# Optimization experiments

Hardware: AMD Instinct MI355X
Metric: run time of the kernel (lower is better)

Reference implementation:

```python
import jax, jax.numpy as jnp
import numpy as np

NUM_NEG_PAIRS = 64
NUM_NEG_INDICES_FOR_LOSS = 16
B, C, H, W = 1, 64, 768, 768
HW = H * W


def setup_inputs() -> dict:
    key = jax.random.key(0)
    k1, k2, k3, k4 = jax.random.split(key, 4)
    feats1 = jax.random.normal(k1, (B, C, H, W), dtype=jnp.float32)
    feats2 = jax.random.normal(k2, (B, C, H, W), dtype=jnp.float32)
    positive_pairs = jax.random.randint(k3, (64, 2), 0, HW, dtype=jnp.int64 if jax.config.jax_enable_x64 else jnp.int32)
    negative_indices = jax.random.randint(k4, (NUM_NEG_PAIRS,), 0, HW, dtype=jnp.int64 if jax.config.jax_enable_x64 else jnp.int32)
    return {"feats1": feats1, "feats2": feats2,
            "positive_pairs": positive_pairs,
            "negative_indices": negative_indices}


def reference(feats1, feats2, positive_pairs, negative_indices):
    # feats1/feats2: [1, C, H, W] -> flatten to [C, HW] (matches .view(C, -1) with B=1)
    f1 = feats1.reshape(C, -1)
    f2 = feats2.reshape(C, -1)
    sel = f1[:, negative_indices]                      # [C, P]
    # squared L2 distance of each selected feature vs all HW locations of feats2
    # ||a-b||^2 = ||a||^2 + ||b||^2 - 2 a.b  (ReLU as in original; dist is nonneg)
    d = (jnp.sum(sel * sel, axis=0)[:, None]
         + jnp.sum(f2 * f2, axis=0)[None, :]
         - 2.0 * jnp.einsum('cp,cn->pn', sel, f2))     # [P, HW]
    d = jax.nn.relu(d)
    # NOTE: the original's mask-exclusion check compares FLOAT distance values
    # against an INT index mask (`dist[...].item() in mask`), which is never true
    # for continuous features, so the effective math is: take the K smallest
    # distances per negative, negate, and average.
    smallest = -jax.lax.top_k(-d, NUM_NEG_INDICES_FOR_LOSS)[0]   # [P, K] smallest dists
    negative_loss = jnp.mean(-smallest, axis=1)                   # [P]
    return jnp.mean(negative_loss)
```

## Files before the change

kernel.cpp:

```cpp
#include <hip/hip_runtime.h>
#include <cstdint>

#define CD 64
#define HWD 589824
#define K1_BLOCKS 1536
#define K1_WAVES (K1_BLOCKS * 4)
#define TPW 3
#define K1_ROWS K1_WAVES
#define FMAXV 3.402823466e+38f

typedef float f32x16 __attribute__((ext_vector_type(16)));
typedef short bf16x8 __attribute__((ext_vector_type(8)));

__device__ __forceinline__ short f2bf(float f) {
    unsigned u = __float_as_uint(f);
    u = u + 0x7FFFu + ((u >> 16) & 1u);
    return (short)(u >> 16);
}

__device__ __forceinline__ void ins4(float4& t, float x) {
    if (x < t.w) {
        if (x < t.z) { t.w = t.z;
            if (x < t.y) { t.z = t.y;
                if (x < t.x) { t.y = t.x; t.x = x; } else t.y = x;
            } else t.z = x;
        } else t.w = x;
    }
}

__device__ __forceinline__ void tile_dist(
    const float* __restrict__ fp,
    const bf16x8* __restrict__ sf0, const bf16x8* __restrict__ sf1,
    int lh, f32x16& acc0, f32x16& acc1, float& fs)
{
    fs = 0.f;
#pragma unroll
    for (int i = 0; i < 16; ++i) { acc0[i] = 0.f; acc1[i] = 0.f; }
#pragma unroll
    for (int ks = 0; ks < 4; ++ks) {
        float av[8];
#pragma unroll
        for (int j = 0; j < 8; ++j)
            av[j] = fp[(long)(16 * ks + 8 * lh + j) * HWD];
        bf16x8 af;
#pragma unroll
        for (int j = 0; j < 8; ++j) {
            fs += av[j] * av[j];
            af[j] = f2bf(av[j]);
        }
        acc0 = __builtin_amdgcn_mfma_f32_32x32x16_bf16(af, sf0[ks], acc0, 0, 0, 0);
        acc1 = __builtin_amdgcn_mfma_f32_32x32x16_bf16(af, sf1[ks], acc1, 0, 0, 0);
    }
    fs += __shfl_xor(fs, 32);
}

__global__ __launch_bounds__(64) void kA_pack(
    const float* __restrict__ f1, const int* __restrict__ nidx,
    short* __restrict__ sel_bf, float* __restrict__ sel2,
    unsigned* __restrict__ ticket)
{
    const int p = blockIdx.x, k = threadIdx.x;
    if (p == 0 && k == 0) *ticket = 0u;
    float v = f1[(long)k * HWD + nidx[p]];
    float s = v * v;
#pragma unroll
    for (int off = 32; off; off >>= 1) s += __shfl_xor(s, off);
    sel_bf[p * CD + k] = f2bf(v);
    if (k == 0) sel2[p] = s;
}

__global__ __launch_bounds__(256) void k1_topk(
    const float* __restrict__ f2, const short* __restrict__ sel_bf,
    const float* __restrict__ sel2, float4* __restrict__ cells)
{
    const int tid = threadIdx.x;
    const int lane = tid & 63, wid = tid >> 6;
    const int l31 = lane & 31, lh = lane >> 5;
    const int gw = blockIdx.x * 4 + wid;

    bf16x8 sf0[4], sf1[4];
#pragma unroll
    for (int ks = 0; ks < 4; ++ks) {
        sf0[ks] = *(const bf16x8*)(sel_bf + l31 * CD + 16 * ks + 8 * lh);
        sf1[ks] = *(const bf16x8*)(sel_bf + (l31 + 32) * CD + 16 * ks + 8 * lh);
    }
    const float sel20 = sel2[l31], sel21 = sel2[l31 + 32];

    float4 t = make_float4(FMAXV, FMAXV, FMAXV, FMAXV);
    float4 u = t;

#pragma unroll
    for (int tt = 0; tt < TPW; ++tt) {
        const long n0 = (long)(gw * TPW + tt) * 32;
        f32x16 a0, a1; float fs;
        tile_dist(f2 + n0 + l31, sf0, sf1, lh, a0, a1, fs);

#pragma unroll
        for (int i = 0; i < 16; ++i) {
            int r = (i & 3) + 8 * (i >> 2) + 4 * lh;
            float fr2 = __shfl(fs, r);
            ins4(t, fmaxf(sel20 + fr2 - 2.f * a0[i], 0.f));
            ins4(u, fmaxf(sel21 + fr2 - 2.f * a1[i], 0.f));
        }
    }

    {
        float4 o;
        o.x = __shfl_xor(t.x, 32); o.y = __shfl_xor(t.y, 32);
        o.z = __shfl_xor(t.z, 32); o.w = __shfl_xor(t.w, 32);
        ins4(t, o.x); ins4(t, o.y); ins4(t, o.z); ins4(t, o.w);
        o.x = __shfl_xor(u.x, 32); o.y = __shfl_xor(u.y, 32);
        o.z = __shfl_xor(u.z, 32); o.w = __shfl_xor(u.w, 32);
        ins4(u, o.x); ins4(u, o.y); ins4(u, o.z); ins4(u, o.w);
    }
    if (lh == 0) {
        cells[(long)gw * CD + l31]      = t;
        cells[(long)gw * CD + l31 + 32] = u;
    }
}

__global__ __launch_bounds__(1024) void k2_sel(
    const float4* __restrict__ cells, float* __restrict__ partial,
    unsigned* __restrict__ ticket, float* __restrict__ out)
{
    const int p = blockIdx.x;
    const int tid = threadIdx.x;
    const int lane = tid & 63, wid = tid >> 6;
    __shared__ unsigned long long wmin[16];

    float4 t = make_float4(FMAXV, FMAXV, FMAXV, FMAXV);
#pragma unroll
    for (int q = 0; q < K1_ROWS / 1024; ++q) {
        float4 b = cells[(long)(tid + q * 1024) * CD + p];
        ins4(t, b.x); ins4(t, b.y); ins4(t, b.z); ins4(t, b.w);
    }

    float sum = 0.f;
    for (int rd = 0; rd < 16; ++rd) {
        unsigned long long key =
            ((unsigned long long)__float_as_uint(t.x) << 32) | (unsigned)tid;
#pragma unroll
        for (int off = 32; off; off >>= 1) {
            unsigned long long o = __shfl_xor(key, off);
            if (o < key) key = o;
        }
        if (lane == 0) wmin[wid] = key;
        __syncthreads();
        unsigned long long gk = wmin[0];
#pragma unroll
        for (int w = 1; w < 16; ++w) if (wmin[w] < gk) gk = wmin[w];
        sum += __uint_as_float((unsigned)(gk >> 32));
        if ((unsigned)(gk & 0xFFFFFFFFu) == (unsigned)tid) {
            t.x = t.y; t.y = t.z; t.z = t.w; t.w = FMAXV;
        }
        __syncthreads();
    }

    if (tid == 0) {
        partial[p] = sum;
        __threadfence();
        unsigned tk = atomicAdd(ticket, 1u);
        if (tk == CD - 1) {
            __threadfence();
            float s = 0.f;
            const volatile float* vp = partial;
            for (int q = 0; q < CD; ++q) s += vp[q];
            out[0] = -s / 1024.0f;
        }
    }
}

extern "C" void kernel_launch(void* const* d_in, const int* in_sizes, int n_in,
                              void* d_out, int out_size, void* d_ws, size_t ws_size,
                              hipStream_t stream)
{
    const float* f1   = (const float*)d_in[0];
    const float* f2   = (const float*)d_in[1];
    const int*   nidx = (const int*)d_in[3];
    float* out = (float*)d_out;

    float4*   cells   = (float4*)d_ws;
    short*    sel_bf  = (short*)(cells + (long)K1_ROWS * CD);
    float*    sel2    = (float*)(sel_bf + CD * CD);
    float*    partial = sel2 + CD;
    unsigned* ticket  = (unsigned*)(partial + CD);

    kA_pack<<<CD,         64, 0, stream>>>(f1, nidx, sel_bf, sel2, ticket);
    k1_topk<<<K1_BLOCKS, 256, 0, stream>>>(f2, sel_bf, sel2, cells);
    k2_sel <<<CD,       1024, 0, stream>>>(cells, partial, ticket, out);
}
```

Baseline: 85.67 us.

## Stage feats2 tiles through LDS with coalesced float4 loads and register prefetch

The top-k kernel now has each block cooperatively load 64x128 tiles of feats2 with float4 coalesced loads into LDS, prefetching the next tile into registers while the current one is processed with MFMA. This replaces the per-lane strided scalar global loads. The grid shrinks to 1152 blocks processing 4 tiles each, and the reduction kernel is adjusted for the new row count. It adds block barriers and LDS traffic in exchange for wider, better-coalesced global reads.

```diff
diff --git a/kernel.cpp b/kernel.cpp
--- a/kernel.cpp
+++ b/kernel.cpp
@@ -3,10 +3,9 @@
 
 #define CD 64
 #define HWD 589824
-#define K1_BLOCKS 1536
-#define K1_WAVES (K1_BLOCKS * 4)
-#define TPW 3
-#define K1_ROWS K1_WAVES
+#define K1_BLOCKS 1152
+#define TPB 4
+#define K1_ROWS (K1_BLOCKS * 4)
 #define FMAXV 3.402823466e+38f
 
 typedef float f32x16 __attribute__((ext_vector_type(16)));
@@ -28,32 +27,6 @@
     }
 }
 
-__device__ __forceinline__ void tile_dist(
-    const float* __restrict__ fp,
-    const bf16x8* __restrict__ sf0, const bf16x8* __restrict__ sf1,
-    int lh, f32x16& acc0, f32x16& acc1, float& fs)
-{
-    fs = 0.f;
-#pragma unroll
-    for (int i = 0; i < 16; ++i) { acc0[i] = 0.f; acc1[i] = 0.f; }
-#pragma unroll
-    for (int ks = 0; ks < 4; ++ks) {
-        float av[8];
-#pragma unroll
-        for (int j = 0; j < 8; ++j)
-            av[j] = fp[(long)(16 * ks + 8 * lh + j) * HWD];
-        bf16x8 af;
-#pragma unroll
-        for (int j = 0; j < 8; ++j) {
-            fs += av[j] * av[j];
-            af[j] = f2bf(av[j]);
-        }
-        acc0 = __builtin_amdgcn_mfma_f32_32x32x16_bf16(af, sf0[ks], acc0, 0, 0, 0);
-        acc1 = __builtin_amdgcn_mfma_f32_32x32x16_bf16(af, sf1[ks], acc1, 0, 0, 0);
-    }
-    fs += __shfl_xor(fs, 32);
-}
-
 __global__ __launch_bounds__(64) void kA_pack(
     const float* __restrict__ f1, const int* __restrict__ nidx,
     short* __restrict__ sel_bf, float* __restrict__ sel2,
@@ -73,10 +46,14 @@
     const float* __restrict__ f2, const short* __restrict__ sel_bf,
     const float* __restrict__ sel2, float4* __restrict__ cells)
 {
+    __shared__ float lds[CD][128];
     const int tid = threadIdx.x;
     const int lane = tid & 63, wid = tid >> 6;
     const int l31 = lane & 31, lh = lane >> 5;
-    const int gw = blockIdx.x * 4 + wid;
+    const long nb = (long)blockIdx.x * (TPB * 128);
+
+    const int srow = tid >> 5;
+    const int scol = (tid & 31) * 4;
 
     bf16x8 sf0[4], sf1[4];
 #pragma unroll
@@ -86,14 +63,50 @@
     }
     const float sel20 = sel2[l31], sel21 = sel2[l31 + 32];
 
+    float4 st[8];
+#pragma unroll
+    for (int i = 0; i < 8; ++i)
+        st[i] = *(const float4*)(f2 + (long)(8 * i + srow) * HWD + nb + scol);
+    __builtin_amdgcn_sched_barrier(0);
+#pragma unroll
+    for (int i = 0; i < 8; ++i)
+        *(float4*)&lds[8 * i + srow][scol] = st[i];
+
     float4 t = make_float4(FMAXV, FMAXV, FMAXV, FMAXV);
     float4 u = t;
 
 #pragma unroll
-    for (int tt = 0; tt < TPW; ++tt) {
-        const long n0 = (long)(gw * TPW + tt) * 32;
-        f32x16 a0, a1; float fs;
-        tile_dist(f2 + n0 + l31, sf0, sf1, lh, a0, a1, fs);
+    for (int tt = 0; tt < TPB; ++tt) {
+        if (tt + 1 < TPB) {
+#pragma unroll
+            for (int i = 0; i < 8; ++i)
+                st[i] = *(const float4*)(f2 + (long)(8 * i + srow) * HWD
+                                         + nb + (long)(tt + 1) * 128 + scol);
+            __builtin_amdgcn_sched_barrier(0);
+        }
+        asm volatile("s_waitcnt lgkmcnt(0)" ::: "memory");
+        __builtin_amdgcn_sched_barrier(0);
+        __builtin_amdgcn_s_barrier();
+        __builtin_amdgcn_sched_barrier(0);
+
+        const int col = wid * 32 + l31;
+        float fs = 0.f;
+        f32x16 a0, a1;
+#pragma unroll
+        for (int i = 0; i < 16; ++i) { a0[i] = 0.f; a1[i] = 0.f; }
+#pragma unroll
+        for (int ks = 0; ks < 4; ++ks) {
+            bf16x8 af;
+#pragma unroll
+            for (int j = 0; j < 8; ++j) {
+                float v = lds[16 * ks + 8 * lh + j][col];
+                fs += v * v;
+                af[j] = f2bf(v);
+            }
+            a0 = __builtin_amdgcn_mfma_f32_32x32x16_bf16(af, sf0[ks], a0, 0, 0, 0);
+            a1 = __builtin_amdgcn_mfma_f32_32x32x16_bf16(af, sf1[ks], a1, 0, 0, 0);
+        }
+        fs += __shfl_xor(fs, 32);
 
 #pragma unroll
         for (int i = 0; i < 16; ++i) {
@@ -101,6 +114,17 @@
             float fr2 = __shfl(fs, r);
             ins4(t, fmaxf(sel20 + fr2 - 2.f * a0[i], 0.f));
             ins4(u, fmaxf(sel21 + fr2 - 2.f * a1[i], 0.f));
+        }
+
+        asm volatile("s_waitcnt lgkmcnt(0)" ::: "memory");
+        __builtin_amdgcn_sched_barrier(0);
+        __builtin_amdgcn_s_barrier();
+        __builtin_amdgcn_sched_barrier(0);
+
+        if (tt + 1 < TPB) {
+#pragma unroll
+            for (int i = 0; i < 8; ++i)
+                *(float4*)&lds[8 * i + srow][scol] = st[i];
         }
     }
 
@@ -114,6 +138,7 @@
         ins4(u, o.x); ins4(u, o.y); ins4(u, o.z); ins4(u, o.w);
     }
     if (lh == 0) {
+        const int gw = blockIdx.x * 4 + wid;
         cells[(long)gw * CD + l31]      = t;
         cells[(long)gw * CD + l31 + 32] = u;
     }
@@ -130,8 +155,12 @@
 
     float4 t = make_float4(FMAXV, FMAXV, FMAXV, FMAXV);
 #pragma unroll
-    for (int q = 0; q < K1_ROWS / 1024; ++q) {
+    for (int q = 0; q < 4; ++q) {
         float4 b = cells[(long)(tid + q * 1024) * CD + p];
+        ins4(t, b.x); ins4(t, b.y); ins4(t, b.z); ins4(t, b.w);
+    }
+    if (tid < K1_ROWS - 4096) {
+        float4 b = cells[(long)(tid + 4096) * CD + p];
         ins4(t, b.x); ins4(t, b.y); ins4(t, b.z); ins4(t, b.w);
     }
 
```

After: 84.37 us. No clear change (-1.5%).
